# Optimization experiments

Hardware: AMD Instinct MI355X
Metric: run time of the kernel (lower is better)

## Reference

```python
import jax, jax.numpy as jnp
import numpy as np
import math

D_MODEL = 2048
NUM_HEADS = 16
HEAD_DIM = D_MODEL // NUM_HEADS  # 128
B, S = 2, 2048


def setup_inputs() -> dict:
    key = jax.random.key(0)
    ks = jax.random.split(key, 11)
    s_in = 1.0 / math.sqrt(D_MODEL)
    return {
        "query": jax.random.normal(ks[0], (B, S, D_MODEL), dtype=jnp.float32),
        "key": jax.random.normal(ks[1], (B, S, D_MODEL), dtype=jnp.float32),
        "value": jax.random.normal(ks[2], (B, S, D_MODEL), dtype=jnp.float32),
        "Wq": jax.random.normal(ks[3], (D_MODEL, D_MODEL), dtype=jnp.float32) * s_in,
        "bq": jnp.zeros((D_MODEL,), dtype=jnp.float32),
        "Wk": jax.random.normal(ks[4], (D_MODEL, HEAD_DIM), dtype=jnp.float32) * s_in,
        "bk": jnp.zeros((HEAD_DIM,), dtype=jnp.float32),
        "Wv": jax.random.normal(ks[5], (D_MODEL, HEAD_DIM), dtype=jnp.float32) * s_in,
        "bv": jnp.zeros((HEAD_DIM,), dtype=jnp.float32),
        "Wo": jax.random.normal(ks[6], (D_MODEL, D_MODEL), dtype=jnp.float32) * s_in,
        "bo": jnp.zeros((D_MODEL,), dtype=jnp.float32),
    }


def reference(query, key, value, Wq, bq, Wk, bk, Wv, bv, Wo, bo):
    b, s, d_model = query.shape
    h, d = NUM_HEADS, HEAD_DIM
    # Projections: Q has h heads, K/V have a single shared head (MQA)
    Q = (query @ Wq + bq).reshape(b, s, h, d).transpose(0, 2, 1, 3)  # [b,h,s,d]
    K = key @ Wk + bk      # [b,s,d]
    V = value @ Wv + bv    # [b,s,d]
    scale = 1.0 / math.sqrt(d)
    # broadcast single K head over all h query heads
    scores = jnp.einsum('bhqd,bkd->bhqk', Q, K) * scale  # [b,h,s,s]
    weights = jax.nn.softmax(scores, axis=-1)
    attn = jnp.einsum('bhqk,bkd->bhqd', weights, V)      # [b,h,s,d]
    attn = attn.transpose(0, 2, 1, 3).reshape(b, s, d_model)
    return attn @ Wo + bo
```

## Files before the change

### kernel.cpp

```cpp
#include <hip/hip_runtime.h>


typedef unsigned short u16;
typedef __attribute__((ext_vector_type(8))) short bf16x8;
typedef __attribute__((ext_vector_type(4))) short bf16x4;
typedef __attribute__((ext_vector_type(4))) float f32x4;

#define D_MODEL 2048
#define SEQ     2048
#define NH      16
#define HD      128
#define BK      32

__device__ __forceinline__ u16 f2bf(float f){
  union { float f; unsigned u; } v; v.f = f;
  unsigned r = (v.u + 0x7FFFu + ((v.u >> 16) & 1u)) >> 16;
  return (u16)r;
}

#if __has_builtin(__builtin_amdgcn_cvt_pk_bf16_f32)
__device__ __forceinline__ unsigned pack2bf(float a, float b){
  auto v = __builtin_amdgcn_cvt_pk_bf16_f32(a, b);
  unsigned u; __builtin_memcpy(&u, &v, 4); return u;
}
#else
__device__ __forceinline__ unsigned pack2bf(float a, float b){
  return (unsigned)f2bf(a) | ((unsigned)f2bf(b) << 16);
}
#endif

__device__ __forceinline__ void gll16(const void* g, void* l){
  __builtin_amdgcn_global_load_lds(
      (const __attribute__((address_space(1))) void*)g,
      (__attribute__((address_space(3))) void*)l, 16, 0, 0);
}

__global__ __launch_bounds__(256) void prep_kernel(
    const float4* __restrict__ qa, const float4* __restrict__ ka, const float4* __restrict__ va,
    ushort4* __restrict__ oq, ushort4* __restrict__ ok, ushort4* __restrict__ ov,
    const float* __restrict__ Wq, const float* __restrict__ Wo,
    const float* __restrict__ Wk, const float* __restrict__ Wv,
    u16* __restrict__ WqT, u16* __restrict__ WoT,
    u16* __restrict__ WkT, u16* __restrict__ WvT){
  __shared__ float tt[32][33];
  int bid = blockIdx.x;
  if (bid < 8192){
    int i = bid*256 + threadIdx.x;
    float4 a = qa[i], b = ka[i], c = va[i];
    ushort4 ra, rb, rc;
    ra.x=f2bf(a.x); ra.y=f2bf(a.y); ra.z=f2bf(a.z); ra.w=f2bf(a.w);
    rb.x=f2bf(b.x); rb.y=f2bf(b.y); rb.z=f2bf(b.z); rb.w=f2bf(b.w);
    rc.x=f2bf(c.x); rc.y=f2bf(c.y); rc.z=f2bf(c.z); rc.w=f2bf(c.w);
    oq[i]=ra; ok[i]=rb; ov[i]=rc;
    return;
  }
  int id = bid - 8192;
  const float* in; u16* outp; int C, bx, by;
  if (id < 4096)      { in=Wq; outp=WqT; C=2048; bx=id&63;        by=id>>6; }
  else if (id < 8192) { id-=4096; in=Wo; outp=WoT; C=2048; bx=id&63; by=id>>6; }
  else if (id < 8448) { id-=8192; in=Wk; outp=WkT; C=128;  bx=id&3;  by=id>>2; }
  else                { id-=8448; in=Wv; outp=WvT; C=128;  bx=id&3;  by=id>>2; }
  const int R = 2048;
  int c0 = bx*32, r0 = by*32;
  int tx = threadIdx.x & 31, ty = threadIdx.x >> 5;
  #pragma unroll
  for (int k=0;k<4;k++) tt[ty+k*8][tx] = in[(size_t)(r0+ty+k*8)*C + c0+tx];
  __syncthreads();
  #pragma unroll
  for (int k=0;k<4;k++) outp[(size_t)(c0+ty+k*8)*R + r0+tx] = f2bf(tt[tx][ty+k*8]);
}

__device__ __forceinline__ void gemm_core_3p(
    const u16* __restrict__ A, const u16* __restrict__ BT,
    int lda, int ldb, int m0, int n0, int kbeg, int kend,
    u16* As, u16* Bs, f32x4 acc[4][4])
{
  const int t = threadIdx.x;
  const int w = t >> 6, l = t & 63;
  const int wr = w >> 1, wc = w & 1;
  const int c16 = l & 15, q = l >> 4;
  const int srow = l >> 2;
  const int sc   = ((l & 3) ^ ((l >> 3) & 3)) * 8;

  int aoff[4], boff[4];
  #pragma unroll
  for (int mt=0;mt<4;mt++){
    int row = wr*64 + mt*16 + c16;
    aoff[mt] = row*BK + ((q ^ ((row>>1)&3))*8);
  }
  #pragma unroll
  for (int nt=0;nt<4;nt++){
    int row = wc*64 + nt*16 + c16;
    boff[nt] = row*BK + ((q ^ ((row>>1)&3))*8);
  }

  auto issue = [&](int k0, int buf){
    u16* Ad = As + buf*4096;
    u16* Bd = Bs + buf*4096;
    #pragma unroll
    for (int half=0; half<2; half++){
      int r = half*64 + w*16 + srow;
      gll16(A  + (size_t)(m0+r)*lda + k0 + sc, Ad + (half*64 + w*16)*BK);
      gll16(BT + (size_t)(n0+r)*ldb + k0 + sc, Bd + (half*64 + w*16)*BK);
    }
  };

  const int n = (kend - kbeg) / BK;
  issue(kbeg, 0);
  issue(kbeg + BK, 1);
  int bi = 0;
  for (int i = 0; i < n; i++){
    if (i + 1 < n) asm volatile("s_waitcnt vmcnt(4)" ::: "memory");
    else           asm volatile("s_waitcnt vmcnt(0)" ::: "memory");
    __builtin_amdgcn_s_barrier();
    if (i + 2 < n){
      int nb = bi + 2; if (nb >= 3) nb -= 3;
      issue(kbeg + (i+2)*BK, nb);
    }
    const u16* Ab = As + bi*4096;
    const u16* Bb = Bs + bi*4096;
    bf16x8 af[4], bfr[4];
    #pragma unroll
    for (int mt=0;mt<4;mt++) af[mt]  = *(const bf16x8*)(Ab + aoff[mt]);
    #pragma unroll
    for (int nt=0;nt<4;nt++) bfr[nt] = *(const bf16x8*)(Bb + boff[nt]);
    #pragma unroll
    for (int mt=0;mt<4;mt++)
      #pragma unroll
      for (int nt=0;nt<4;nt++)
        acc[mt][nt] = __builtin_amdgcn_mfma_f32_16x16x32_bf16(af[mt], bfr[nt], acc[mt][nt], 0,0,0);
    bi++; if (bi == 3) bi = 0;
  }
}

__global__ __launch_bounds__(256) void proj_kernel(
    const u16* __restrict__ kb, const u16* __restrict__ vb,
    const u16* __restrict__ WkT, const u16* __restrict__ WvT,
    float* __restrict__ part)
{
  __shared__ u16 As[3*4096], Bs[3*4096];
  f32x4 acc[4][4];
  f32x4 z = {0.f,0.f,0.f,0.f};
  #pragma unroll
  for (int i=0;i<4;i++) for (int j=0;j<4;j++) acc[i][j] = z;
  const int t = threadIdx.x, w = t>>6, l = t&63, wr = w>>1, wc = w&1, c16 = l&15, q = l>>4;
  int id = blockIdx.x;
  int zi = id & 3, nb = (id >> 2) & 1, mi = id >> 3;
  const u16* Am = nb ? vb  : kb;
  const u16* Bm = nb ? WvT : WkT;
  gemm_core_3p(Am, Bm, 2048, 2048, mi*128, 0, zi*512, zi*512+512, As, Bs, acc);
  float* dst = part + (size_t)(zi*2 + nb)*524288;
  #pragma unroll
  for (int mt=0;mt<4;mt++)
    #pragma unroll
    for (int nt=0;nt<4;nt++){
      int col = wc*64 + nt*16 + c16;
      #pragma unroll
      for (int r=0;r<4;r++){
        int row = mi*128 + wr*64 + mt*16 + q*4 + r;
        dst[(size_t)row*128 + col] = acc[mt][nt][r];
      }
    }
}

__global__ __launch_bounds__(256) void oproj_kernel(
    const u16* __restrict__ A, const u16* __restrict__ BT, const float* __restrict__ bias,
    float* __restrict__ C)
{
  __shared__ u16 As[3*4096], Bs[3*4096];
  f32x4 acc[4][4];
  f32x4 z = {0.f,0.f,0.f,0.f};
  #pragma unroll
  for (int i=0;i<4;i++) for (int j=0;j<4;j++) acc[i][j] = z;
  int id = blockIdx.x;
  int x = id & 7, j = id >> 3;
  int m0 = (x*4 + (j & 3))*128, n0 = (j >> 2)*128;
  gemm_core_3p(A, BT, 2048, 2048, m0, n0, 0, 2048, As, Bs, acc);
  const int t = threadIdx.x, w = t>>6, l = t&63, wr = w>>1, wc = w&1, c16 = l&15, q = l>>4;
  #pragma unroll
  for (int mt=0;mt<4;mt++)
    #pragma unroll
    for (int nt=0;nt<4;nt++){
      int col = n0 + wc*64 + nt*16 + c16;
      float bv = bias[col];
      #pragma unroll
      for (int r=0;r<4;r++){
        int row = m0 + wr*64 + mt*16 + q*4 + r;
        C[(size_t)row*D_MODEL + col] = acc[mt][nt][r] + bv;
      }
    }
}

__global__ __launch_bounds__(256) void kv_reduce_kernel(
    const float* __restrict__ part, const float* __restrict__ bk, const float* __restrict__ bv,
    u16* __restrict__ Kp, u16* __restrict__ VpT){
  int idx = blockIdx.x*256 + threadIdx.x;
  int d = idx & 127, sg = idx >> 7;
  float ka = 0.f, va = 0.f;
  #pragma unroll
  for (int zi=0; zi<4; zi++){
    ka += part[(size_t)(zi*2+0)*524288 + idx];
    va += part[(size_t)(zi*2+1)*524288 + idx];
  }
  Kp[idx] = f2bf(ka + bk[d]);
  int b = sg >> 11, sl = sg & 2047;
  VpT[(size_t)b*262144 + (size_t)d*2048 + sl] = f2bf(va + bv[d]);
}

__global__ __launch_bounds__(512, 2) void attn_kernel(
    const u16* __restrict__ qb, const u16* __restrict__ WqT, const float* __restrict__ bq,
    const u16* __restrict__ Kp, const u16* __restrict__ VpT, u16* __restrict__ attnb){
  __shared__ u16 lds[65536];
  const int t = threadIdx.x;
  const int w = t >> 6, l = t & 63;
  const int c16 = l & 15, q = l >> 4;

  const int qt = blockIdx.x;
  const int bh = blockIdx.y;
  const int b = bh >> 4, h = bh & 15;

  f32x4 o[2][8];
  f32x4 z4 = {0.f,0.f,0.f,0.f};
  #pragma unroll
  for (int qs=0;qs<2;qs++) for (int dt=0;dt<8;dt++) o[qs][dt] = z4;

  {
    const u16* Aq = qb  + (size_t)(b*SEQ + qt*256)*D_MODEL;
    const u16* Bw = WqT + (size_t)(h*HD)*D_MODEL;
    u16* As = lds;
    u16* Bs = lds + 24576;
    const int srow = l >> 2;
    const int sc   = ((l & 3) ^ ((l >> 3) & 3)) * 8;
    auto issueQ = [&](int k0, int buf){
      u16* Ad = As + buf*8192;
      u16* Bd = Bs + buf*4096;
      #pragma unroll
      for (int half=0; half<2; half++){
        int r = half*128 + w*16 + srow;
        gll16(Aq + (size_t)r*D_MODEL + k0 + sc, Ad + (half*128 + w*16)*BK);
      }
      { int r = w*16 + srow;
        gll16(Bw + (size_t)r*D_MODEL + k0 + sc, Bd + (w*16)*BK); }
    };
    issueQ(0, 0);
    issueQ(BK, 1);
    int bi = 0;
    const int swz = (q ^ ((c16>>1)&3))*8;
    for (int i = 0; i < 64; i++){
      if (i + 1 < 64) asm volatile("s_waitcnt vmcnt(3)" ::: "memory");
      else            asm volatile("s_waitcnt vmcnt(0)" ::: "memory");
      __builtin_amdgcn_s_barrier();
      if (i + 2 < 64){
        int nb2 = bi + 2; if (nb2 >= 3) nb2 -= 3;
        issueQ((i+2)*BK, nb2);
      }
      const u16* Ab = As + bi*8192;
      const u16* Bb = Bs + bi*4096;
      bf16x8 qrow0 = *(const bf16x8*)(Ab + (w*32      + c16)*BK + swz);
      bf16x8 qrow1 = *(const bf16x8*)(Ab + (w*32 + 16 + c16)*BK + swz);
      bf16x8 wcol[8];
      #pragma unroll
      for (int dt=0;dt<8;dt++)
        wcol[dt] = *(const bf16x8*)(Bb + (dt*16 + c16)*BK + swz);
      __builtin_amdgcn_s_setprio(1);
      #pragma unroll
      for (int dt=0;dt<8;dt++){
        o[0][dt] = __builtin_amdgcn_mfma_f32_16x16x32_bf16(wcol[dt], qrow0, o[0][dt], 0,0,0);
        o[1][dt] = __builtin_amdgcn_mfma_f32_16x16x32_bf16(wcol[dt], qrow1, o[1][dt], 0,0,0);
      }
      __builtin_amdgcn_s_setprio(0);
      bi++; if (bi == 3) bi = 0;
    }
    __syncthreads();
    #pragma unroll
    for (int qs=0;qs<2;qs++){
      int row = w*32 + qs*16 + c16;
      #pragma unroll
      for (int dt=0;dt<8;dt++){
        float4 bb = *(const float4*)(bq + h*HD + dt*16 + q*4);
        uint2 val;
        val.x = pack2bf(o[qs][dt][0]+bb.x, o[qs][dt][1]+bb.y);
        val.y = pack2bf(o[qs][dt][2]+bb.z, o[qs][dt][3]+bb.w);
        int ch = dt*2 + (q>>1);
        *(uint2*)(lds + row*128 + ((ch ^ c16)&15)*8 + (q&1)*4) = val;
      }
    }
    __syncthreads();
  }

  bf16x8 qf[2][4];
  #pragma unroll
  for (int qs=0;qs<2;qs++)
    #pragma unroll
    for (int kk=0;kk<4;kk++){
      int ch = kk*4 + q;
      qf[qs][kk] = *(const bf16x8*)(lds + (w*32 + qs*16 + c16)*128 + ((ch ^ c16)&15)*8);
    }
  __syncthreads();
  #pragma unroll
  for (int qs=0;qs<2;qs++) for (int dt=0;dt<8;dt++) o[qs][dt] = z4;

  const u16* Kbase = Kp  + (size_t)(b*SEQ)*HD;
  const u16* Vbase = VpT + (size_t)b*HD*SEQ;
  const int sr = w*4 + (l >> 4);
  #pragma unroll
  for (int j=0;j<4;j++){
    int r = j*32 + sr;
    int g = (l & 15) ^ (r & 15);
    gll16(Kbase + (size_t)r*HD + g*8, lds + j*4096 + w*512);
  }
  #pragma unroll
  for (int j=0;j<4;j++){
    int d = j*32 + sr;
    int g = (l & 15) ^ (d & 15);
    gll16(Vbase + (size_t)d*SEQ + g*8, lds + 32768 + j*4096 + w*512);
  }
  __syncthreads();

  float mrow[2] = {-1e30f, -1e30f};
  float lrow[2] = {0.f, 0.f};
  const float cs = 0.08838834764831845f * 1.4426950408889634f;

  for (int kt = 0; kt < 16; kt++){
    const int p = kt & 1;
    if (kt < 15){
      u16* Kd = lds + (p^1)*16384;
      u16* Vd = lds + 32768 + (p^1)*16384;
      #pragma unroll
      for (int j=0;j<4;j++){
        int r = j*32 + sr;
        int g = (l & 15) ^ (r & 15);
        gll16(Kbase + (size_t)((kt+1)*128 + r)*HD + g*8, Kd + j*4096 + w*512);
      }
      #pragma unroll
      for (int j=0;j<4;j++){
        int d = j*32 + sr;
        int g = (l & 15) ^ (d & 15);
        gll16(Vbase + (size_t)d*SEQ + (kt+1)*128 + g*8, Vd + j*4096 + w*512);
      }
    }
    const u16* Ks = lds + p*16384;
    const u16* Vs = lds + 32768 + p*16384;

    f32x4 s[2][8];
    __builtin_amdgcn_s_setprio(1);
    #pragma unroll
    for (int kt8=0; kt8<8; kt8++){
      {
        bf16x8 kf = *(const bf16x8*)(Ks + (kt8*16 + c16)*128 + ((q ^ c16) & 15)*8);
        s[0][kt8] = __builtin_amdgcn_mfma_f32_16x16x32_bf16(kf, qf[0][0], z4, 0,0,0);
        s[1][kt8] = __builtin_amdgcn_mfma_f32_16x16x32_bf16(kf, qf[1][0], z4, 0,0,0);
      }
      #pragma unroll
      for (int kk=1;kk<4;kk++){
        int ch = kk*4 + q;
        bf16x8 kf = *(const bf16x8*)(Ks + (kt8*16 + c16)*128 + ((ch ^ c16) & 15)*8);
        s[0][kt8] = __builtin_amdgcn_mfma_f32_16x16x32_bf16(kf, qf[0][kk], s[0][kt8], 0,0,0);
        s[1][kt8] = __builtin_amdgcn_mfma_f32_16x16x32_bf16(kf, qf[1][kk], s[1][kt8], 0,0,0);
      }
    }
    __builtin_amdgcn_s_setprio(0);

    float vmax[2];
    #pragma unroll
    for (int qs=0; qs<2; qs++){
      float xx[8];
      #pragma unroll
      for (int kt8=0;kt8<8;kt8++)
        xx[kt8] = fmaxf(fmaxf(s[qs][kt8][0],s[qs][kt8][1]), fmaxf(s[qs][kt8][2],s[qs][kt8][3]));
      float vm = fmaxf(fmaxf(fmaxf(xx[0],xx[1]),fmaxf(xx[2],xx[3])),
                       fmaxf(fmaxf(xx[4],xx[5]),fmaxf(xx[6],xx[7])));
      vm = fmaxf(vm, __shfl_xor(vm, 16));
      vm = fmaxf(vm, __shfl_xor(vm, 32));
      vmax[qs] = vm;
    }
    bool upd = ((vmax[0]-mrow[0])*cs > 8.f) || ((vmax[1]-mrow[1])*cs > 8.f);
    if (__any(upd)){
      #pragma unroll
      for (int qs=0; qs<2; qs++){
        float mnew = fmaxf(mrow[qs], vmax[qs]);
        float a = exp2f((mrow[qs]-mnew)*cs);
        mrow[qs] = mnew; lrow[qs] *= a;
        #pragma unroll
        for (int dt=0;dt<8;dt++)
          #pragma unroll
          for (int r=0;r<4;r++) o[qs][dt][r] *= a;
      }
    }
    union PU { unsigned u[4]; bf16x8 v; } P32[2][4];
    #pragma unroll
    for (int qs=0; qs<2; qs++){
      float mc = mrow[qs]*cs;
      float rsum = 0.f;
      #pragma unroll
      for (int kt8=0;kt8<8;kt8++){
        float p0 = exp2f(__builtin_fmaf(s[qs][kt8][0], cs, -mc));
        float p1 = exp2f(__builtin_fmaf(s[qs][kt8][1], cs, -mc));
        float p2 = exp2f(__builtin_fmaf(s[qs][kt8][2], cs, -mc));
        float p3 = exp2f(__builtin_fmaf(s[qs][kt8][3], cs, -mc));
        s[qs][kt8][0]=p0; s[qs][kt8][1]=p1; s[qs][kt8][2]=p2; s[qs][kt8][3]=p3;
        rsum += (p0+p1)+(p2+p3);
      }
      rsum += __shfl_xor(rsum, 16);
      rsum += __shfl_xor(rsum, 32);
      lrow[qs] += rsum;
      #pragma unroll
      for (int kb=0;kb<4;kb++){
        P32[qs][kb].u[0] = pack2bf(s[qs][2*kb][0],   s[qs][2*kb][1]);
        P32[qs][kb].u[1] = pack2bf(s[qs][2*kb][2],   s[qs][2*kb][3]);
        P32[qs][kb].u[2] = pack2bf(s[qs][2*kb+1][0], s[qs][2*kb+1][1]);
        P32[qs][kb].u[3] = pack2bf(s[qs][2*kb+1][2], s[qs][2*kb+1][3]);
      }
    }

    __builtin_amdgcn_s_setprio(1);
    #pragma unroll
    for (int kb=0; kb<4; kb++){
      int ca = 4*kb + (q>>1);
      int cb = ca + 2;
      #pragma unroll
      for (int dt=0; dt<8; dt++){
        int d = dt*16 + c16;
        union VU { bf16x4 hh[2]; bf16x8 v; } vf;
        vf.hh[0] = *(const bf16x4*)(Vs + d*128 + ((ca ^ c16) & 15)*8 + (q&1)*4);
        vf.hh[1] = *(const bf16x4*)(Vs + d*128 + ((cb ^ c16) & 15)*8 + (q&1)*4);
        o[0][dt] = __builtin_amdgcn_mfma_f32_16x16x32_bf16(vf.v, P32[0][kb].v, o[0][dt], 0,0,0);
        o[1][dt] = __builtin_amdgcn_mfma_f32_16x16x32_bf16(vf.v, P32[1][kb].v, o[1][dt], 0,0,0);
      }
    }
    __builtin_amdgcn_s_setprio(0);
    __syncthreads();
  }

  #pragma unroll
  for (int qs=0;qs<2;qs++){
    float inv = 1.f / lrow[qs];
    int qrow = qt*256 + w*32 + qs*16 + c16;
    u16* dst = attnb + ((size_t)(b*SEQ) + qrow)*D_MODEL + h*HD + q*4;
    #pragma unroll
    for (int dt=0;dt<8;dt++){
      ushort4 pk;
      pk.x = f2bf(o[qs][dt][0]*inv);
      pk.y = f2bf(o[qs][dt][1]*inv);
      pk.z = f2bf(o[qs][dt][2]*inv);
      pk.w = f2bf(o[qs][dt][3]*inv);
      *(ushort4*)(dst + dt*16) = pk;
    }
  }
}

extern "C" void kernel_launch(void* const* d_in, const int* in_sizes, int n_in,
                              void* d_out, int out_size, void* d_ws, size_t ws_size,
                              hipStream_t stream) {
  (void)in_sizes; (void)n_in; (void)out_size; (void)ws_size;
  const float* query = (const float*)d_in[0];
  const float* key   = (const float*)d_in[1];
  const float* value = (const float*)d_in[2];
  const float* Wq    = (const float*)d_in[3];
  const float* bq    = (const float*)d_in[4];
  const float* Wk    = (const float*)d_in[5];
  const float* bk    = (const float*)d_in[6];
  const float* Wv    = (const float*)d_in[7];
  const float* bv    = (const float*)d_in[8];
  const float* Wo    = (const float*)d_in[9];
  const float* bo    = (const float*)d_in[10];
  float* out = (float*)d_out;

  char* W = (char*)d_ws;
  u16*  qb     = (u16*) (W + 0);
  u16*  kb     = (u16*) (W + 16777216);
  u16*  vb     = (u16*) (W + 33554432);
  u16*  WqT    = (u16*) (W + 50331648);
  u16*  WoT    = (u16*) (W + 58720256);
  u16*  WkT    = (u16*) (W + 67108864);
  u16*  WvT    = (u16*) (W + 67633152);
  u16*  Kp     = (u16*) (W + 84934656);
  u16*  VpT    = (u16*) (W + 85983232);
  u16*  attnb  = (u16*) (W + 87031808);
  float* kvpart= (float*)(W + 103809024);

  prep_kernel<<<16896, 256, 0, stream>>>(
      (const float4*)query, (const float4*)key, (const float4*)value,
      (ushort4*)qb, (ushort4*)kb, (ushort4*)vb,
      Wq, Wo, Wk, Wv, WqT, WoT, WkT, WvT);
  proj_kernel<<<256, 256, 0, stream>>>(kb, vb, WkT, WvT, kvpart);
  kv_reduce_kernel<<<2048, 256, 0, stream>>>(kvpart, bk, bv, Kp, VpT);
  attn_kernel<<<dim3(8,32), 512, 0, stream>>>(qb, WqT, bq, Kp, VpT, attnb);
  oproj_kernel<<<512, 256, 0, stream>>>(attnb, WoT, bo, out);
}
```

Before: 385.7 us.

## Shrink output-projection tiles to 128x64 with double-buffered inline GEMM loop

The output projection no longer calls the shared triple-buffered 128x128 GEMM core. It runs its own loop with 128x64 tiles, double-buffered LDS, half the accumulators and a launch bound of 4 blocks per CU, and the grid doubles to 1024 blocks. The aim is more resident waves and better CU fill on the 4096x2048 output GEMM. In exchange each block reuses its A tile over fewer columns, so A is loaded from global memory twice as often, and there is only one prefetch stage to hide latency.

```diff
diff --git a/kernel.cpp b/kernel.cpp
--- a/kernel.cpp
+++ b/kernel.cpp
@@ -163,25 +163,74 @@
     }
 }
 
-__global__ __launch_bounds__(256) void oproj_kernel(
+__global__ __launch_bounds__(256, 4) void oproj_kernel(
     const u16* __restrict__ A, const u16* __restrict__ BT, const float* __restrict__ bias,
     float* __restrict__ C)
 {
-  __shared__ u16 As[3*4096], Bs[3*4096];
-  f32x4 acc[4][4];
+  __shared__ u16 As[2*4096], Bs[2*2048];
+  f32x4 acc[4][2];
   f32x4 z = {0.f,0.f,0.f,0.f};
   #pragma unroll
-  for (int i=0;i<4;i++) for (int j=0;j<4;j++) acc[i][j] = z;
+  for (int i=0;i<4;i++) for (int j=0;j<2;j++) acc[i][j] = z;
+  const int t = threadIdx.x;
+  const int w = t >> 6, l = t & 63;
+  const int wr = w >> 1, wc = w & 1;
+  const int c16 = l & 15, q = l >> 4;
+  const int srow = l >> 2;
+  const int sc   = ((l & 3) ^ ((l >> 3) & 3)) * 8;
+
   int id = blockIdx.x;
   int x = id & 7, j = id >> 3;
-  int m0 = (x*4 + (j & 3))*128, n0 = (j >> 2)*128;
-  gemm_core_3p(A, BT, 2048, 2048, m0, n0, 0, 2048, As, Bs, acc);
-  const int t = threadIdx.x, w = t>>6, l = t&63, wr = w>>1, wc = w&1, c16 = l&15, q = l>>4;
+  int m0 = (x*4 + (j & 3))*128;
+  int n0 = (j >> 2)*64;
+
+  int aoff[4], boff[2];
+  #pragma unroll
+  for (int mt=0;mt<4;mt++){
+    int row = wr*64 + mt*16 + c16;
+    aoff[mt] = row*BK + ((q ^ ((row>>1)&3))*8);
+  }
+  #pragma unroll
+  for (int nt=0;nt<2;nt++){
+    int row = wc*32 + nt*16 + c16;
+    boff[nt] = row*BK + ((q ^ ((row>>1)&3))*8);
+  }
+
+  auto issue = [&](int k0, int buf){
+    u16* Ad = As + buf*4096;
+    u16* Bd = Bs + buf*2048;
+    #pragma unroll
+    for (int half=0; half<2; half++){
+      int r = half*64 + w*16 + srow;
+      gll16(A + (size_t)(m0+r)*2048 + k0 + sc, Ad + (half*64 + w*16)*BK);
+    }
+    { int r = w*16 + srow;
+      gll16(BT + (size_t)(n0+r)*2048 + k0 + sc, Bd + (w*16)*BK); }
+  };
+
+  issue(0, 0);
+  for (int i = 0; i < 64; i++){
+    __syncthreads();
+    if (i+1 < 64) issue((i+1)*BK, (i+1)&1);
+    const u16* Ab = As + (i&1)*4096;
+    const u16* Bb = Bs + (i&1)*2048;
+    bf16x8 af[4], bfr[2];
+    #pragma unroll
+    for (int mt=0;mt<4;mt++) af[mt]  = *(const bf16x8*)(Ab + aoff[mt]);
+    #pragma unroll
+    for (int nt=0;nt<2;nt++) bfr[nt] = *(const bf16x8*)(Bb + boff[nt]);
+    #pragma unroll
+    for (int mt=0;mt<4;mt++)
+      #pragma unroll
+      for (int nt=0;nt<2;nt++)
+        acc[mt][nt] = __builtin_amdgcn_mfma_f32_16x16x32_bf16(af[mt], bfr[nt], acc[mt][nt], 0,0,0);
+  }
+
   #pragma unroll
   for (int mt=0;mt<4;mt++)
     #pragma unroll
-    for (int nt=0;nt<4;nt++){
-      int col = n0 + wc*64 + nt*16 + c16;
+    for (int nt=0;nt<2;nt++){
+      int col = n0 + wc*32 + nt*16 + c16;
       float bv = bias[col];
       #pragma unroll
       for (int r=0;r<4;r++){
@@ -486,5 +535,5 @@
   proj_kernel<<<256, 256, 0, stream>>>(kb, vb, WkT, WvT, kvpart);
   kv_reduce_kernel<<<2048, 256, 0, stream>>>(kvpart, bk, bv, Kp, VpT);
   attn_kernel<<<dim3(8,32), 512, 0, stream>>>(qb, WqT, bq, Kp, VpT, attnb);
-  oproj_kernel<<<512, 256, 0, stream>>>(attnb, WoT, bo, out);
-}
+  oproj_kernel<<<1024, 256, 0, stream>>>(attnb, WoT, bo, out);
+}
```

Result: no change. 390.1 us (+1.1%).
